# Kernel tuning notes

Measured on AMD Instinct MI355X. Metric: run time of the kernel, lower is better.

The kernel has to match this reference:

```python
import jax, jax.numpy as jnp
import numpy as np
import math

T = 120      # frame_num == audio_len == max_seq_len
D = 64       # hidden_layer_size
H = 2        # n_head
DH = D // H
DFF = 2 * D
DOUT = 31
PERIOD = 10
EPS = 1e-5
NEG = -1e9
SCALE = 1.0 / math.sqrt(DH)
SLOPES = (1.0 / 16.0, 1.0 / 256.0)  # ALiBi slopes for n_head=2


def _pe():
    # PeriodicPositionalEncoding: sinusoid over one period, tiled
    pos = jnp.arange(PERIOD, dtype=jnp.float32)[:, None]
    div = jnp.exp(jnp.arange(0, D, 2, dtype=jnp.float32) * (-math.log(10000.0) / D))
    s, c = jnp.sin(pos * div), jnp.cos(pos * div)
    pe = jnp.stack([s, c], axis=-1).reshape(PERIOD, D)  # interleave sin/cos
    return jnp.tile(pe, (T // PERIOD + 1, 1))[:T]


def _alibi_mask():
    # causal mask + ALiBi bias: alibi[i,j] = -slope * floor((i-j)/period) for j<=i
    slopes = jnp.array(SLOPES, dtype=jnp.float32)
    i = jnp.arange(T)[:, None]
    j = jnp.arange(T)[None, :]
    rel = ((i - j) // PERIOD).astype(jnp.float32)
    return jnp.where(j <= i, -slopes[:, None, None] * rel, NEG)  # [H,T,T]


def _ln(x, g, b):
    m = x.mean(-1, keepdims=True)
    v = ((x - m) ** 2).mean(-1, keepdims=True)
    return (x - m) / jnp.sqrt(v + EPS) * g + b


def setup_inputs() -> dict:
    key = jax.random.key(0)
    ks = iter(jax.random.split(key, 32))
    n = lambda shape, s=0.05: jax.random.normal(next(ks), shape, dtype=jnp.float32) * s
    inp = {
        'audio': jax.random.normal(next(ks), (1, T, 1024), dtype=jnp.float32),
        'W_audio': n((D, 1024)), 'b_audio': n((D,)),
        'obj_W': n((D, 5)),
        'Wq': n((D, D)), 'bq': n((D,)), 'Wk': n((D, D)), 'bk': n((D,)),
        'Wv': n((D, D)), 'bv': n((D,)), 'Wo': n((D, D)), 'bo': n((D,)),
        'Wv2': n((D, D)), 'bv2': n((D,)), 'Wo2': n((D, D)), 'bo2': n((D,)),
        'g1': jnp.ones((D,)), 'be1': jnp.zeros((D,)),
        'g2': jnp.ones((D,)), 'be2': jnp.zeros((D,)),
        'g3': jnp.ones((D,)), 'be3': jnp.zeros((D,)),
        'W1': n((DFF, D)), 'c1': n((DFF,)), 'W2': n((D, DFF)), 'c2': n((D,)),
        'Wr': n((DOUT, D)), 'br': n((DOUT,)), 'Wm': n((D, DOUT)), 'bm': n((D,)),
    }
    return inp


def _forward(audio, W_audio, b_audio, obj_W, Wq, bq, Wk, bk, Wv, bv, Wo, bo,
             Wv2, bv2, Wo2, bo2, g1, be1, g2, be2, g3, be3,
             W1, c1, W2, c2, Wr, br, Wm, bm):
    mem = audio[0] @ W_audio.T + b_audio          # [S,D], S == T
    style = obj_W[:, 0]                            # obj_vector @ [1,0,0,0,0]
    pe = _pe()
    mask = _alibi_mask()
    slopes = jnp.array(SLOPES, dtype=jnp.float32)
    jarr = jnp.arange(T)

    # enc_dec_mask leaves exactly one memory key per target row (anti-diagonal
    # from the end); the feedback row t at step t always attends memory[-1],
    # so its cross-attn output is just the projected value of the last frame.
    cross_last = (mem[-1] @ Wv2.T + bv2) @ Wo2.T + bo2  # [D]

    def step(emb, t):
        # decode only the last row (row t) of the growing sequence; 1-layer
        # post-norm decoder => row t depends only on input rows 0..t.
        x = emb + pe                                 # PPE over prefix
        xq = jnp.take(x, t, axis=0)                  # [D]
        q = (xq @ Wq.T + bq).reshape(H, DH)
        k = (x @ Wk.T + bk).reshape(T, H, DH)
        v = (x @ Wv.T + bv).reshape(T, H, DH)
        bias = jnp.where(jarr <= t,
                         -slopes[:, None] * ((t - jarr) // PERIOD).astype(jnp.float32),
                         NEG)                        # [H,T]
        sc = jnp.einsum('hd,shd->hs', q, k) * SCALE + bias
        a = jax.nn.softmax(sc, axis=-1)
        sa = jnp.einsum('hs,shd->hd', a, v).reshape(D) @ Wo.T + bo
        h1 = _ln(xq + sa, g1, be1)
        h2 = _ln(h1 + cross_last, g2, be2)
        h3 = _ln(h2 + jax.nn.relu(h2 @ W1.T + c1) @ W2.T + c2, g3, be3)
        new = (h3 @ Wr.T + br) @ Wm.T + bm + style   # vertice_map(vertice_map_r(.)) + style
        emb = jax.lax.dynamic_update_slice(emb, new[None, :], (t + 1, 0))
        return emb, None

    emb0 = jnp.zeros((T, D), audio.dtype).at[0].set(style)
    emb, _ = jax.lax.scan(step, emb0, jnp.arange(T - 1))

    # final full-length decode (last loop iteration of the torch module)
    x = emb + pe
    q = (x @ Wq.T + bq).reshape(T, H, DH)
    k = (x @ Wk.T + bk).reshape(T, H, DH)
    v = (x @ Wv.T + bv).reshape(T, H, DH)
    sc = jnp.einsum('thd,shd->hts', q, k) * SCALE + mask
    a = jax.nn.softmax(sc, axis=-1)
    sa = jnp.einsum('hts,shd->thd', a, v).reshape(T, D) @ Wo.T + bo
    h1 = _ln(x + sa, g1, be1)
    # at length T with S == T the enc_dec_mask aligns target row j <-> memory row j
    cross = (mem @ Wv2.T + bv2) @ Wo2.T + bo2
    h2 = _ln(h1 + cross, g2, be2)
    h3 = _ln(h2 + jax.nn.relu(h2 @ W1.T + c1) @ W2.T + c2, g3, be3)
    return (h3 @ Wr.T + br)[None]                    # [1,T,31]


def reference(audio, W_audio, b_audio, obj_W, Wq, bq, Wk, bk, Wv, bv, Wo, bo,
              Wv2, bv2, Wo2, bo2, g1, be1, g2, be2, g3, be3,
              W1, c1, W2, c2, Wr, br, Wm, bm):
    return _forward(audio, W_audio, b_audio, obj_W, Wq, bq, Wk, bk, Wv, bv, Wo, bo,
                    Wv2, bv2, Wo2, bo2, g1, be1, g2, be2, g3, be3,
                    W1, c1, W2, c2, Wr, br, Wm, bm)
```

## Files before the change

kernel.cpp:

```cpp
#include <hip/hip_runtime.h>

typedef unsigned short u16;
typedef unsigned int   u32;
typedef _Float16 f16;
typedef f16 h2 __attribute__((ext_vector_type(2)));
typedef f16 h4 __attribute__((ext_vector_type(4)));
typedef f16 h8 __attribute__((ext_vector_type(8)));

#define T_    120
#define D_    64
#define DOUT_ 31
#define KROW_ 68
#define VROW_ 132

#if defined(__has_builtin)
#if __has_builtin(__builtin_amdgcn_fdot2)
#define DOT2(a,b,c) __builtin_amdgcn_fdot2((a),(b),(c),false)
#endif
#endif
#ifndef DOT2
#define DOT2(a,b,c) ((float)(a).x*(float)(b).x + ((float)(a).y*(float)(b).y + (c)))
#endif
#define SHV(x,i,j) __builtin_shufflevector((x),(x),(i),(j))

__device__ __forceinline__ h2 pk(float a, float b){
#if defined(__has_builtin) && __has_builtin(__builtin_amdgcn_cvt_pkrtz)
  return __builtin_bit_cast(h2, __builtin_amdgcn_cvt_pkrtz(a, b));
#else
  h2 r; r.x = (f16)a; r.y = (f16)b; return r;
#endif
}
__device__ __forceinline__ float2 bp2(u32 u){
  float2 r; r.x = __uint_as_float(u << 16); r.y = __uint_as_float(u & 0xffff0000u); return r;
}
__device__ __forceinline__ u16 f2bu(float f){
  u32 u = __float_as_uint(f);
  u32 r = u + 0x7fffu + ((u >> 16) & 1u);
  return (u16)(r >> 16);
}
__device__ __forceinline__ u16 f2h16(float x){
  f16 v = (f16)x; u16 r; __builtin_memcpy(&r, &v, 2); return r;
}
__device__ __forceinline__ float fast_rcp(float x){
#if defined(__has_builtin) && __has_builtin(__builtin_amdgcn_rcpf)
  return __builtin_amdgcn_rcpf(x);
#else
  return 1.f / x;
#endif
}
#define WSYNC() do{ __asm__ __volatile__("" ::: "memory"); __builtin_amdgcn_wave_barrier(); }while(0)

__device__ __forceinline__ float dpp_sum(float x){
  int t;
  t = __builtin_amdgcn_update_dpp(0, __float_as_int(x), 0x111, 0xf, 0xf, true); x += __int_as_float(t);
  t = __builtin_amdgcn_update_dpp(0, __float_as_int(x), 0x112, 0xf, 0xf, true); x += __int_as_float(t);
  t = __builtin_amdgcn_update_dpp(0, __float_as_int(x), 0x114, 0xf, 0xf, true); x += __int_as_float(t);
  t = __builtin_amdgcn_update_dpp(0, __float_as_int(x), 0x118, 0xf, 0xf, true); x += __int_as_float(t);
  t = __builtin_amdgcn_update_dpp(0, __float_as_int(x), 0x142, 0xf, 0xf, true); x += __int_as_float(t);
  t = __builtin_amdgcn_update_dpp(0, __float_as_int(x), 0x143, 0xf, 0xf, true); x += __int_as_float(t);
  return __int_as_float(__builtin_amdgcn_readlane(__float_as_int(x), 63));
}
__device__ __forceinline__ float dpp_max_pos(float x){
  int t;
  t = __builtin_amdgcn_update_dpp(0, __float_as_int(x), 0x111, 0xf, 0xf, true); x = fmaxf(x, __int_as_float(t));
  t = __builtin_amdgcn_update_dpp(0, __float_as_int(x), 0x112, 0xf, 0xf, true); x = fmaxf(x, __int_as_float(t));
  t = __builtin_amdgcn_update_dpp(0, __float_as_int(x), 0x114, 0xf, 0xf, true); x = fmaxf(x, __int_as_float(t));
  t = __builtin_amdgcn_update_dpp(0, __float_as_int(x), 0x118, 0xf, 0xf, true); x = fmaxf(x, __int_as_float(t));
  t = __builtin_amdgcn_update_dpp(0, __float_as_int(x), 0x142, 0xf, 0xf, true); x = fmaxf(x, __int_as_float(t));
  t = __builtin_amdgcn_update_dpp(0, __float_as_int(x), 0x143, 0xf, 0xf, true); x = fmaxf(x, __int_as_float(t));
  return __int_as_float(__builtin_amdgcn_readlane(__float_as_int(x), 63));
}
__device__ __forceinline__ float pe_val(int row, int i){
  const float coef = -0.28782313662425574f;
  int p = row % 10;
  float dv  = __expf((float)(i >> 1) * coef);
  float ang = (float)p * dv;
  return (i & 1) ? __cosf(ang) : __sinf(ang);
}
__device__ __forceinline__ void loadrow32(h2* dst, const float* row){
  #pragma unroll
  for (int r = 0; r < 16; ++r){
    float4 f = ((const float4*)row)[r];
    dst[2*r]   = pk(f.x, f.y);
    dst[2*r+1] = pk(f.z, f.w);
  }
}

__global__ __launch_bounds__(256) void k_pre0(const float* __restrict__ audio,
                                              const float* __restrict__ Wa, const float* __restrict__ ba,
                                              const float* __restrict__ Wv2, const float* __restrict__ bv2,
                                              const float* __restrict__ Wo2, const float* __restrict__ bo2,
                                              const float* __restrict__ Wo, const float* __restrict__ W1,
                                              const float* __restrict__ W2, const float* __restrict__ Wr,
                                              const float* __restrict__ Wm, const float* __restrict__ br,
                                              const float* __restrict__ bm,
                                              float* __restrict__ cross, float* __restrict__ Ms,
                                              float* __restrict__ bMv,
                                              u16* __restrict__ wob, u16* __restrict__ w1b,
                                              u16* __restrict__ w2b, u16* __restrict__ wrb){
  const int tid = threadIdx.x;
  __shared__ float ash[1024];
  __shared__ float msh[64], tsh[64];
  for (int i = tid; i < 1024; i += 256) ash[i] = audio[119*1024 + i];
  for (int i = tid; i < 4096; i += 256) wob[i] = f2bu(Wo[i]);
  for (int i = tid; i < 8192; i += 256){ w1b[i] = f2bu(W1[i]); w2b[i] = f2bu(W2[i]); }
  for (int i = tid; i < 1984; i += 256) wrb[i] = f2bu(Wr[i]);
  for (int idx = tid; idx < 4096; idx += 256){
    int d = idx >> 6, e = idx & 63;
    float acc = 0.f;
    #pragma unroll
    for (int j = 0; j < 31; ++j) acc += Wm[d*31 + j] * Wr[j*64 + e];
    Ms[idx] = acc;
  }
  if (tid < 64){
    float acc = bm[tid];
    #pragma unroll
    for (int j = 0; j < 31; ++j) acc += Wm[tid*31 + j] * br[j];
    bMv[tid] = acc;
  }
  __syncthreads();
  const int w = tid >> 6, lane = tid & 63;
  for (int d = w*16; d < w*16 + 16; ++d){
    const float4* row = (const float4*)(Wa + d*1024);
    float acc = 0.f;
    #pragma unroll
    for (int m = 0; m < 4; ++m){
      float4 wp = row[lane + 64*m];
      int j = 4*(lane + 64*m);
      acc += wp.x*ash[j] + wp.y*ash[j+1] + wp.z*ash[j+2] + wp.w*ash[j+3];
    }
    acc = dpp_sum(acc);
    if (lane == 0) msh[d] = acc + ba[d];
  }
  __syncthreads();
  if (tid < 64){
    const float4* r1 = (const float4*)(Wv2 + tid*64);
    float a = bv2[tid];
    #pragma unroll
    for (int j = 0; j < 16; ++j){ float4 p = r1[j]; a += p.x*msh[4*j] + p.y*msh[4*j+1] + p.z*msh[4*j+2] + p.w*msh[4*j+3]; }
    tsh[tid] = a;
  }
  __syncthreads();
  if (tid < 64){
    const float4* r2 = (const float4*)(Wo2 + tid*64);
    float c = bo2[tid];
    #pragma unroll
    for (int j = 0; j < 16; ++j){ float4 p = r2[j]; c += p.x*tsh[4*j] + p.y*tsh[4*j+1] + p.z*tsh[4*j+2] + p.w*tsh[4*j+3]; }
    cross[119*64 + tid] = c;
  }
}

__global__ __launch_bounds__(128, 1) void k_main(
    const float* __restrict__ audio,
    const float* __restrict__ Wa, const float* __restrict__ ba,
    const float* __restrict__ Wv2, const float* __restrict__ bv2,
    const float* __restrict__ Wo2, const float* __restrict__ bo2,
    const float* __restrict__ objW,
    const float* __restrict__ Wq, const float* __restrict__ bq,
    const float* __restrict__ Wk, const float* __restrict__ bk,
    const float* __restrict__ Wv, const float* __restrict__ bv,
    const float* __restrict__ Wo, const float* __restrict__ bo,
    const float* __restrict__ g1, const float* __restrict__ be1,
    const float* __restrict__ g2, const float* __restrict__ be2,
    const float* __restrict__ g3, const float* __restrict__ be3,
    const float* __restrict__ W1, const float* __restrict__ c1,
    const float* __restrict__ W2, const float* __restrict__ c2,
    const float* __restrict__ Ms, const float* __restrict__ bMv,
    float* __restrict__ cross,
    u16* __restrict__ xw16, u16* __restrict__ Kw16, u16* __restrict__ Vw16)
{
  __shared__ __align__(16) f16 KcS[128*KROW_];
  __shared__ __align__(16) f16 VcS[D_*VROW_];
  __shared__ __align__(16) f16 xwS[T_*D_];
  __shared__ __align__(16) f16 sch[256];
  __shared__ __align__(16) f16 xh[64], qh[64], h2h[64], h3h[64];
  __shared__ __align__(16) f16 at2h[64];
  __shared__ __align__(16) f16 fsh[128];
  __shared__ float pP0[64], pP1[64];
  __shared__ float ivP[2];
  __shared__ float pe_tab[640];

  const int tid = threadIdx.x;

  if (blockIdx.x != 119){
    float* ash = (float*)KcS;
    float* msh = (float*)VcS;
    float* tsh = msh + 64;
    const int b = blockIdx.x;
    for (int idx = tid; idx < 1024; idx += 128) ash[idx] = audio[b*1024 + idx];
    __syncthreads();
    const int w = tid >> 6, lane = tid & 63;
    for (int d = w*32; d < w*32 + 32; ++d){
      const float4* row = (const float4*)(Wa + d*1024);
      float acc = 0.f;
      #pragma unroll
      for (int m = 0; m < 4; ++m){
        float4 wp = row[lane + 64*m];
        int j = 4*(lane + 64*m);
        acc += wp.x*ash[j] + wp.y*ash[j+1] + wp.z*ash[j+2] + wp.w*ash[j+3];
      }
      acc = dpp_sum(acc);
      if (lane == 0) msh[d] = acc + ba[d];
    }
    __syncthreads();
    if (tid < 64){
      const float4* r1 = (const float4*)(Wv2 + tid*64);
      float a = bv2[tid];
      #pragma unroll
      for (int j = 0; j < 16; ++j){ float4 p = r1[j]; a += p.x*msh[4*j] + p.y*msh[4*j+1] + p.z*msh[4*j+2] + p.w*msh[4*j+3]; }
      tsh[tid] = a;
    }
    __syncthreads();
    if (tid < 64){
      const float4* r2 = (const float4*)(Wo2 + tid*64);
      float c = bo2[tid];
      #pragma unroll
      for (int j = 0; j < 16; ++j){ float4 p = r2[j]; c += p.x*tsh[4*j] + p.y*tsh[4*j+1] + p.z*tsh[4*j+2] + p.w*tsh[4*j+3]; }
      cross[b*64 + tid] = c;
    }
    return;
  }

  const int i = tid & 63;
  const int hh = tid >> 6;
  const bool w1w = hh != 0;

  h2 A[32], B[32], C[32], D[32], G[32], E[32];
  float biasA=0.f, biasB=0.f, bo_r=0.f, c1r=0.f, c2_r=0.f, cls_r=0.f;
  float g1r=0.f,b1r=0.f,g2r=0.f,b2r=0.f;
  float mg_r=0.f, u_r=0.f;
  float x_r;

  {
    const int qi = hh*32 + (i & 31);
    if (i < 32){ loadrow32(A, Wq + qi*64); biasA = bq[qi]; }
    else       { loadrow32(A, Wk + qi*64); biasA = bk[qi]; }
    loadrow32(B, Wv + qi*64);  biasB = bv[qi];
    loadrow32(C, Wo + i*64);
    loadrow32(D, W1 + (hh*64 + i)*64);
    loadrow32(G, W2 + i*128 + hh*64);
    {
      const float4* mr  = (const float4*)(Ms + i*64);
      const float4* gv  = (const float4*)g3;
      const float4* b3v = (const float4*)be3;
      float mg = 0.f, mb = 0.f;
      #pragma unroll
      for (int r = 0; r < 16; ++r){
        float4 f = mr[r], g = gv[r], b = b3v[r];
        float e0 = f.x*g.x, e1 = f.y*g.y, e2 = f.z*g.z, e3 = f.w*g.w;
        E[2*r]   = pk(e0, e1);
        E[2*r+1] = pk(e2, e3);
        mg += (e0+e1)+(e2+e3);
        mb += f.x*b.x + f.y*b.y + f.z*b.z + f.w*b.w;
      }
      mg_r = mg;
      u_r  = bMv[i] + objW[i*5] + mb;
    }
    c1r = c1[hh*64 + i]; c2_r = c2[i]; bo_r = bo[i];
    g1r = g1[i]; b1r = be1[i]; g2r = g2[i]; b2r = be2[i];
    cls_r = cross[119*64 + i];
  }
  { u32* p = (u32*)KcS; for (int idx = tid; idx < 128*KROW_/2; idx += 128) p[idx] = 0; }
  { u32* p = (u32*)VcS; for (int idx = tid; idx < D_*VROW_/2;  idx += 128) p[idx] = 0; }
  for (int idx = tid; idx < 640; idx += 128) pe_tab[idx] = pe_val(idx >> 6, idx & 63);
  {
    float x0 = objW[i*5] + pe_val(0, i);
    x_r = x0;
    xh[i] = (f16)x0;
    if (w1w) xwS[i] = (f16)x0;
  }
  __syncthreads();

  int pp = 1;
  const float slope = hh ? 0.00390625f : 0.0625f;
  for (int t = 0; t < T_-1; ++t){
    float e0r, e1r;
    h8 xr[8];
    {
      const h8* xv = (const h8*)xh;
      #pragma unroll
      for (int r = 0; r < 8; ++r) xr[r] = xv[r];
      float a0=biasA,a1=0.f,a2=0.f,a3=0.f;
      #pragma unroll
      for (int r = 0; r < 8; ++r){
        h8 x = xr[r];
        a0 = DOT2(A[4*r+0], SHV(x,0,1), a0);
        a1 = DOT2(A[4*r+1], SHV(x,2,3), a1);
        a2 = DOT2(A[4*r+2], SHV(x,4,5), a2);
        a3 = DOT2(A[4*r+3], SHV(x,6,7), a3);
      }
      float qk = (a0+a1)+(a2+a3);
      f16* dst = (i < 32) ? (qh + hh*32 + i) : (KcS + t*KROW_ + hh*32 + (i - 32));
      *dst = (f16)qk;
    }
    WSYNC();
    {
      if (i < 32){
        float v0=biasB,v1=0.f,v2=0.f,v3=0.f;
        #pragma unroll
        for (int r = 0; r < 8; ++r){
          h8 x = xr[r];
          v0 = DOT2(B[4*r+0], SHV(x,0,1), v0); v1 = DOT2(B[4*r+1], SHV(x,2,3), v1);
          v2 = DOT2(B[4*r+2], SHV(x,4,5), v2); v3 = DOT2(B[4*r+3], SHV(x,6,7), v3);
        }
        VcS[(hh*32 + i)*VROW_ + t] = (f16)((v0+v1)+(v2+v3));
      }
      const int j = i;
      const h8* qv = (const h8*)(qh + hh*32);
      const h4* k0 = (const h4*)(KcS + j*KROW_ + hh*32);
      const h4* k1 = (const h4*)(KcS + (j+64)*KROW_ + hh*32);
      float d0a=0.f,d0b=0.f,d1a=0.f,d1b=0.f;
      #pragma unroll
      for (int r = 0; r < 4; ++r){
        h8 q = qv[r];
        h4 ka = k0[2*r], kb = k0[2*r+1], kc = k1[2*r], kd = k1[2*r+1];
        d0a = DOT2(SHV(ka,0,1), SHV(q,0,1), d0a);
        d0b = DOT2(SHV(ka,2,3), SHV(q,2,3), d0b);
        d0a = DOT2(SHV(kb,0,1), SHV(q,4,5), d0a);
        d0b = DOT2(SHV(kb,2,3), SHV(q,6,7), d0b);
        d1a = DOT2(SHV(kc,0,1), SHV(q,0,1), d1a);
        d1b = DOT2(SHV(kc,2,3), SHV(q,2,3), d1b);
        d1a = DOT2(SHV(kd,0,1), SHV(q,4,5), d1a);
        d1b = DOT2(SHV(kd,2,3), SHV(q,6,7), d1b);
      }
      float d0 = d0a + d0b, d1 = d1a + d1b;
      int r0 = (t - j) / 10, r1 = (t - j - 64) / 10;
      float s0 = d0*0.17677669529663687f - slope*(float)r0;
      float s1 = d1*0.17677669529663687f - slope*(float)r1;
      e0r = (j      <= t) ? __expf(fminf(s0, 8.f)) : 0.f;
      e1r = (j + 64 <= t) ? __expf(fminf(s1, 8.f)) : 0.f;
      sch[hh*128 + j]      = (f16)e0r;
      sch[hh*128 + j + 64] = (f16)e1r;
    }
    WSYNC();
    {
      float den = dpp_sum(e0r + e1r);
      float inv_w = fast_rcp(den);
      if (i == 0) ivP[hh] = inv_w;
      const int l5 = i & 31;
      const int d  = hh*32 + l5;
      const int co = (i & 32) ? 64 : 0;
      const h8* av = (const h8*)(sch + hh*128 + co);
      const h4* vv = (const h4*)(VcS + d*VROW_ + co);
      float p0=0.f,p1=0.f,p2=0.f,p3=0.f;
      #pragma unroll
      for (int r = 0; r < 8; ++r){
        h8 a = av[r];
        h4 va = vv[2*r], vb = vv[2*r+1];
        p0 = DOT2(SHV(va,0,1), SHV(a,0,1), p0);
        p1 = DOT2(SHV(va,2,3), SHV(a,2,3), p1);
        p2 = DOT2(SHV(vb,0,1), SHV(a,4,5), p2);
        p3 = DOT2(SHV(vb,2,3), SHV(a,6,7), p3);
      }
      float p = (p0+p1)+(p2+p3);
      p += __shfl_xor(p, 32, 64);
      at2h[hh*32 + l5] = (f16)p;
    }
    __syncthreads();
    float h2v;
    {
      float inv0 = ivP[0], inv1 = ivP[1];
      const h8* pv = (const h8*)at2h;
      float l0=0.f,l1=0.f,q0=0.f,q1=0.f;
      #pragma unroll
      for (int r = 0; r < 4; ++r){
        h8 x = pv[r];
        l0 = DOT2(C[4*r+0], SHV(x,0,1), l0); l1 = DOT2(C[4*r+1], SHV(x,2,3), l1);
        l0 = DOT2(C[4*r+2], SHV(x,4,5), l0); l1 = DOT2(C[4*r+3], SHV(x,6,7), l1);
      }
      #pragma unroll
      for (int r = 4; r < 8; ++r){
        h8 x = pv[r];
        q0 = DOT2(C[4*r+0], SHV(x,0,1), q0); q1 = DOT2(C[4*r+1], SHV(x,2,3), q1);
        q0 = DOT2(C[4*r+2], SHV(x,4,5), q0); q1 = DOT2(C[4*r+3], SHV(x,6,7), q1);
      }
      float sa = bo_r + inv0*(l0+l1) + inv1*(q0+q1);
      float y = x_r + sa;
      float s = dpp_sum(y), s2 = dpp_sum(y*y);
      float m = s*(1.f/64.f), var = fmaxf(s2*(1.f/64.f) - m*m, 0.f);
      float h1 = (y - m)*rsqrtf(var + 1e-5f)*g1r + b1r;
      float z = h1 + cls_r;
      float sz = dpp_sum(z), sz2 = dpp_sum(z*z);
      float mz = sz*(1.f/64.f), vz = fmaxf(sz2*(1.f/64.f) - mz*mz, 0.f);
      h2v = (z - mz)*rsqrtf(vz + 1e-5f)*g2r + b2r;
      h2h[i] = (f16)h2v;
      WSYNC();
      const h8* hv = (const h8*)h2h;
      float a0=c1r, a1=0.f, a2=0.f, a3=0.f;
      #pragma unroll
      for (int r = 0; r < 8; ++r){
        h8 x = hv[r];
        a0 = DOT2(D[4*r+0], SHV(x,0,1), a0);
        a1 = DOT2(D[4*r+1], SHV(x,2,3), a1);
        a2 = DOT2(D[4*r+2], SHV(x,4,5), a2);
        a3 = DOT2(D[4*r+3], SHV(x,6,7), a3);
      }
      fsh[hh*64 + i] = (f16)fmaxf((a0+a1)+(a2+a3), 0.f);
      WSYNC();
      const h8* fv = (const h8*)(fsh + hh*64);
      float f0=0.f, f1=0.f, f2=0.f, f3=0.f;
      #pragma unroll
      for (int r = 0; r < 8; ++r){
        h8 x = fv[r];
        f0 = DOT2(G[4*r+0], SHV(x,0,1), f0);
        f1 = DOT2(G[4*r+1], SHV(x,2,3), f1);
        f2 = DOT2(G[4*r+2], SHV(x,4,5), f2);
        f3 = DOT2(G[4*r+3], SHV(x,6,7), f3);
      }
      float* pP = hh ? pP1 : pP0;
      pP[i] = (f0+f1)+(f2+f3);
    }
    __syncthreads();
    {
      float y3 = h2v + c2_r + pP0[i] + pP1[i];
      h3h[i] = (f16)y3;
      WSYNC();
      const h8* yv3 = (const h8*)h3h;
      h8 yr[8];
      #pragma unroll
      for (int r = 0; r < 8; ++r) yr[r] = yv3[r];
      float s3 = dpp_sum(y3), s32 = dpp_sum(y3*y3);
      float m3 = s3*(1.f/64.f), v3 = fmaxf(s32*(1.f/64.f) - m3*m3, 0.f);
      float invs = rsqrtf(v3 + 1e-5f);
      float m0=0.f, m1=0.f, m2=0.f, mm3=0.f;
      #pragma unroll
      for (int r = 0; r < 8; ++r){
        h8 x = yr[r];
        m0 = DOT2(E[4*r+0], SHV(x,0,1), m0);
        m1 = DOT2(E[4*r+1], SHV(x,2,3), m1);
        m2 = DOT2(E[4*r+2], SHV(x,4,5), m2);
        mm3 = DOT2(E[4*r+3], SHV(x,6,7), mm3);
      }
      float xn = ((m0+m1)+(m2+mm3))*invs + (u_r - m3*invs*mg_r) + pe_tab[pp*64 + i];
      x_r = xn;
      xh[i] = (f16)xn;
      if (w1w) xwS[(t+1)*64 + i] = (f16)xn;
    }
    WSYNC();
    pp = (pp == 9) ? 0 : pp + 1;
  }
  {
    const h8* xv = (const h8*)xh;
    h8 xr[8];
    #pragma unroll
    for (int r = 0; r < 8; ++r) xr[r] = xv[r];
    if (i < 32){
      float v0=biasB,v1=0.f,v2=0.f,v3=0.f;
      #pragma unroll
      for (int r = 0; r < 8; ++r){
        h8 x = xr[r];
        v0 = DOT2(B[4*r+0], SHV(x,0,1), v0);
        v1 = DOT2(B[4*r+1], SHV(x,2,3), v1);
        v2 = DOT2(B[4*r+2], SHV(x,4,5), v2);
        v3 = DOT2(B[4*r+3], SHV(x,6,7), v3);
      }
      Vw16[119*64 + hh*32 + i] = f2h16((v0+v1)+(v2+v3));
    } else {
      float k0=biasA,k1=0.f,k2=0.f,k3=0.f;
      #pragma unroll
      for (int r = 0; r < 8; ++r){
        h8 x = xr[r];
        k0 = DOT2(A[4*r+0], SHV(x,0,1), k0);
        k1 = DOT2(A[4*r+1], SHV(x,2,3), k1);
        k2 = DOT2(A[4*r+2], SHV(x,4,5), k2);
        k3 = DOT2(A[4*r+3], SHV(x,6,7), k3);
      }
      Kw16[119*64 + hh*32 + (i-32)] = f2h16((k0+k1)+(k2+k3));
    }
  }
  __syncthreads();
  {
    const u16* kc = (const u16*)KcS;
    const u16* vc = (const u16*)VcS;
    for (int idx = tid; idx < 119*64; idx += 128){
      int t_ = idx >> 6, d = idx & 63;
      Kw16[idx] = kc[t_*KROW_ + d];
      Vw16[idx] = vc[d*VROW_ + t_];
    }
    const u32* xs32 = (const u32*)xwS;
    for (int idx = tid; idx < T_*D_/2; idx += 128) ((u32*)xw16)[idx] = xs32[idx];
  }
}

__global__ __launch_bounds__(128) void k_final(
    const float* __restrict__ Wq, const float* __restrict__ bq, const float* __restrict__ bo,
    const float* __restrict__ g1, const float* __restrict__ be1,
    const float* __restrict__ g2, const float* __restrict__ be2,
    const float* __restrict__ g3, const float* __restrict__ be3,
    const float* __restrict__ c1, const float* __restrict__ c2, const float* __restrict__ br,
    const u16* __restrict__ wo_b, const u16* __restrict__ w1_b,
    const u16* __restrict__ w2_b, const u16* __restrict__ wr_b,
    const float* __restrict__ cross, const u16* __restrict__ xw16,
    const u16* __restrict__ Kw16, const u16* __restrict__ Vw16,
    float* __restrict__ out)
{
  __shared__ float xs[64], qs[64], at[64], h2s[64], h3s[64], fs[128], sc[256];
  const int irow = blockIdx.x, tid = threadIdx.x;
  const f16* xp = (const f16*)xw16;
  const f16* kp = (const f16*)Kw16;
  const f16* vp = (const f16*)Vw16;
  if (tid < 64) xs[tid] = (float)xp[irow*64 + tid];
  __syncthreads();
  if (tid < 64){
    const float4* wr_ = (const float4*)(Wq + tid*64);
    float acc = bq[tid];
    #pragma unroll
    for (int j = 0; j < 16; ++j){ float4 w = wr_[j]; acc += w.x*xs[4*j] + w.y*xs[4*j+1] + w.z*xs[4*j+2] + w.w*xs[4*j+3]; }
    qs[tid] = acc;
  }
  __syncthreads();
  {
    const int h = tid >> 6, j = tid & 63;
    const float* qh_ = qs + h*32;
    float d0 = 0.f, d1 = 0.f;
    const h4* k0 = (const h4*)(kp + j*64 + h*32);
    #pragma unroll
    for (int w = 0; w < 8; ++w){
      h4 p = k0[w];
      d0 += (float)p.x*qh_[4*w] + (float)p.y*qh_[4*w+1] + (float)p.z*qh_[4*w+2] + (float)p.w*qh_[4*w+3];
    }
    if (j < 56){
      const h4* k1 = (const h4*)(kp + (j+64)*64 + h*32);
      #pragma unroll
      for (int w = 0; w < 8; ++w){
        h4 p = k1[w];
        d1 += (float)p.x*qh_[4*w] + (float)p.y*qh_[4*w+1] + (float)p.z*qh_[4*w+2] + (float)p.w*qh_[4*w+3];
      }
    }
    const float slope = h ? 0.00390625f : 0.0625f;
    float s0 = (j      <= irow) ? d0*0.17677669529663687f - slope*(float)((irow-j)/10)    : -1e30f;
    float s1 = (j + 64 <= irow) ? d1*0.17677669529663687f - slope*(float)((irow-j-64)/10) : -1e30f;
    float m = dpp_max_pos(fmaxf(s0, s1) + 16384.f) - 16384.f;
    float e0 = (j      <= irow) ? __expf(s0 - m) : 0.f;
    float e1 = (j + 64 <= irow) ? __expf(s1 - m) : 0.f;
    float inv = 1.f / dpp_sum(e0 + e1);
    sc[h*128 + j]      = e0*inv;
    sc[h*128 + j + 64] = e1*inv;
  }
  __syncthreads();
  if (tid < 64){
    const float* a = sc + (tid >> 5)*128;
    float a0=0.f,a1=0.f,a2=0.f,a3=0.f;
    #pragma unroll
    for (int jj = 0; jj < 30; ++jj){
      a0 += a[4*jj]   * (float)vp[(4*jj)*64   + tid];
      a1 += a[4*jj+1] * (float)vp[(4*jj+1)*64 + tid];
      a2 += a[4*jj+2] * (float)vp[(4*jj+2)*64 + tid];
      a3 += a[4*jj+3] * (float)vp[(4*jj+3)*64 + tid];
    }
    at[tid] = (a0+a1)+(a2+a3);
  }
  __syncthreads();
  if (tid < 64){
    const u32* orow = (const u32*)(wo_b + tid*64);
    float acc = bo[tid];
    #pragma unroll
    for (int w = 0; w < 32; ++w){ float2 p = bp2(orow[w]); acc += p.x*at[2*w] + p.y*at[2*w+1]; }
    float y = xs[tid] + acc;
    float s = dpp_sum(y), s2 = dpp_sum(y*y);
    float m = s*(1.f/64.f), var = fmaxf(s2*(1.f/64.f) - m*m, 0.f);
    float h1 = (y - m)*rsqrtf(var + 1e-5f)*g1[tid] + be1[tid];
    float z = h1 + cross[irow*64 + tid];
    float sz = dpp_sum(z), sz2 = dpp_sum(z*z);
    float mz = sz*(1.f/64.f), vz = fmaxf(sz2*(1.f/64.f) - mz*mz, 0.f);
    h2s[tid] = (z - mz)*rsqrtf(vz + 1e-5f)*g2[tid] + be2[tid];
  }
  __syncthreads();
  {
    const u32* w1r = (const u32*)(w1_b + tid*64);
    float acc = c1[tid];
    #pragma unroll
    for (int w = 0; w < 32; ++w){ float2 p = bp2(w1r[w]); acc += p.x*h2s[2*w] + p.y*h2s[2*w+1]; }
    fs[tid] = fmaxf(acc, 0.f);
  }
  __syncthreads();
  if (tid < 64){
    const u32* w2r = (const u32*)(w2_b + tid*128);
    float acc = c2[tid];
    #pragma unroll
    for (int w = 0; w < 64; ++w){ float2 p = bp2(w2r[w]); acc += p.x*fs[2*w] + p.y*fs[2*w+1]; }
    float y = h2s[tid] + acc;
    float s = dpp_sum(y), s2 = dpp_sum(y*y);
    float m = s*(1.f/64.f), var = fmaxf(s2*(1.f/64.f) - m*m, 0.f);
    h3s[tid] = (y - m)*rsqrtf(var + 1e-5f)*g3[tid] + be3[tid];
  }
  __syncthreads();
  if (tid < DOUT_){
    const u32* rr = (const u32*)(wr_b + tid*64);
    float acc = br[tid];
    #pragma unroll
    for (int w = 0; w < 32; ++w){ float2 p = bp2(rr[w]); acc += p.x*h3s[2*w] + p.y*h3s[2*w+1]; }
    out[irow*DOUT_ + tid] = acc;
  }
}

extern "C" void kernel_launch(void* const* d_in, const int* in_sizes, int n_in,
                              void* d_out, int out_size, void* d_ws, size_t ws_size,
                              hipStream_t stream){
  const float* audio=(const float*)d_in[0];
  const float* Wa   =(const float*)d_in[1];
  const float* ba   =(const float*)d_in[2];
  const float* objW =(const float*)d_in[3];
  const float* Wq   =(const float*)d_in[4];
  const float* bq   =(const float*)d_in[5];
  const float* Wk   =(const float*)d_in[6];
  const float* bk   =(const float*)d_in[7];
  const float* Wv   =(const float*)d_in[8];
  const float* bv   =(const float*)d_in[9];
  const float* Wo   =(const float*)d_in[10];
  const float* bo   =(const float*)d_in[11];
  const float* Wv2  =(const float*)d_in[12];
  const float* bv2  =(const float*)d_in[13];
  const float* Wo2  =(const float*)d_in[14];
  const float* bo2  =(const float*)d_in[15];
  const float* g1   =(const float*)d_in[16];
  const float* be1  =(const float*)d_in[17];
  const float* g2   =(const float*)d_in[18];
  const float* be2  =(const float*)d_in[19];
  const float* g3   =(const float*)d_in[20];
  const float* be3  =(const float*)d_in[21];
  const float* W1   =(const float*)d_in[22];
  const float* c1   =(const float*)d_in[23];
  const float* W2   =(const float*)d_in[24];
  const float* c2   =(const float*)d_in[25];
  const float* Wr   =(const float*)d_in[26];
  const float* br   =(const float*)d_in[27];
  const float* Wm   =(const float*)d_in[28];
  const float* bm   =(const float*)d_in[29];

  float* ws    = (float*)d_ws;
  float* cross = ws;
  float* Ms    = ws + 7680;
  float* bMv   = ws + 11776;
  u16* xw16 = (u16*)(ws + 11840);
  u16* Kw16 = xw16 + 7680;
  u16* Vw16 = Kw16 + 7680;
  u16* wo_b = Vw16 + 7680;
  u16* w1_b = wo_b + 4096;
  u16* w2_b = w1_b + 8192;
  u16* wr_b = w2_b + 8192;
  float* out = (float*)d_out;

  k_pre0 <<<dim3(1),   dim3(256), 0, stream>>>(audio, Wa, ba, Wv2, bv2, Wo2, bo2,
                                               Wo, W1, W2, Wr, Wm, br, bm,
                                               cross, Ms, bMv, wo_b, w1_b, w2_b, wr_b);
  k_main <<<dim3(120), dim3(128), 0, stream>>>(audio, Wa, ba, Wv2, bv2, Wo2, bo2,
                                               objW, Wq, bq, Wk, bk, Wv, bv, Wo, bo,
                                               g1, be1, g2, be2, g3, be3,
                                               W1, c1, W2, c2, Ms, bMv,
                                               cross, xw16, Kw16, Vw16);
  k_final<<<dim3(120), dim3(128), 0, stream>>>(Wq, bq, bo, g1, be1, g2, be2, g3, be3,
                                               c1, c2, br, wo_b, w1_b, w2_b, wr_b,
                                               cross, xw16, Kw16, Vw16, out);
}
```

Baseline: 381.1 us.

## Fold prep kernel into single-block scan and compute cross rows in final kernel

Removes the separate single-block prep kernel. Its weight conversion, Wm·Wr folding and last-row cross computation move into the single-block scan kernel's prologue. The 119 cross-attention rows that were computed by extra blocks of the main kernel are now computed per row inside the final kernel. The FFN second layer is no longer split across both waves with a partial-sum reduction; each wave holds the full W2 row in registers. This drops one launch and the global cross/Ms buffers, but it lengthens the serial prologue of the scan, where the weight conversion and Wm·Wr product now run on only 128 threads, and it raises register pressure.

```diff
diff --git a/kernel.cpp b/kernel.cpp
--- a/kernel.cpp
+++ b/kernel.cpp
@@ -86,71 +86,7 @@
   }
 }
 
-__global__ __launch_bounds__(256) void k_pre0(const float* __restrict__ audio,
-                                              const float* __restrict__ Wa, const float* __restrict__ ba,
-                                              const float* __restrict__ Wv2, const float* __restrict__ bv2,
-                                              const float* __restrict__ Wo2, const float* __restrict__ bo2,
-                                              const float* __restrict__ Wo, const float* __restrict__ W1,
-                                              const float* __restrict__ W2, const float* __restrict__ Wr,
-                                              const float* __restrict__ Wm, const float* __restrict__ br,
-                                              const float* __restrict__ bm,
-                                              float* __restrict__ cross, float* __restrict__ Ms,
-                                              float* __restrict__ bMv,
-                                              u16* __restrict__ wob, u16* __restrict__ w1b,
-                                              u16* __restrict__ w2b, u16* __restrict__ wrb){
-  const int tid = threadIdx.x;
-  __shared__ float ash[1024];
-  __shared__ float msh[64], tsh[64];
-  for (int i = tid; i < 1024; i += 256) ash[i] = audio[119*1024 + i];
-  for (int i = tid; i < 4096; i += 256) wob[i] = f2bu(Wo[i]);
-  for (int i = tid; i < 8192; i += 256){ w1b[i] = f2bu(W1[i]); w2b[i] = f2bu(W2[i]); }
-  for (int i = tid; i < 1984; i += 256) wrb[i] = f2bu(Wr[i]);
-  for (int idx = tid; idx < 4096; idx += 256){
-    int d = idx >> 6, e = idx & 63;
-    float acc = 0.f;
-    #pragma unroll
-    for (int j = 0; j < 31; ++j) acc += Wm[d*31 + j] * Wr[j*64 + e];
-    Ms[idx] = acc;
-  }
-  if (tid < 64){
-    float acc = bm[tid];
-    #pragma unroll
-    for (int j = 0; j < 31; ++j) acc += Wm[tid*31 + j] * br[j];
-    bMv[tid] = acc;
-  }
-  __syncthreads();
-  const int w = tid >> 6, lane = tid & 63;
-  for (int d = w*16; d < w*16 + 16; ++d){
-    const float4* row = (const float4*)(Wa + d*1024);
-    float acc = 0.f;
-    #pragma unroll
-    for (int m = 0; m < 4; ++m){
-      float4 wp = row[lane + 64*m];
-      int j = 4*(lane + 64*m);
-      acc += wp.x*ash[j] + wp.y*ash[j+1] + wp.z*ash[j+2] + wp.w*ash[j+3];
-    }
-    acc = dpp_sum(acc);
-    if (lane == 0) msh[d] = acc + ba[d];
-  }
-  __syncthreads();
-  if (tid < 64){
-    const float4* r1 = (const float4*)(Wv2 + tid*64);
-    float a = bv2[tid];
-    #pragma unroll
-    for (int j = 0; j < 16; ++j){ float4 p = r1[j]; a += p.x*msh[4*j] + p.y*msh[4*j+1] + p.z*msh[4*j+2] + p.w*msh[4*j+3]; }
-    tsh[tid] = a;
-  }
-  __syncthreads();
-  if (tid < 64){
-    const float4* r2 = (const float4*)(Wo2 + tid*64);
-    float c = bo2[tid];
-    #pragma unroll
-    for (int j = 0; j < 16; ++j){ float4 p = r2[j]; c += p.x*tsh[4*j] + p.y*tsh[4*j+1] + p.z*tsh[4*j+2] + p.w*tsh[4*j+3]; }
-    cross[119*64 + tid] = c;
-  }
-}
-
-__global__ __launch_bounds__(128, 1) void k_main(
+__global__ __launch_bounds__(128, 1) void k_scan(
     const float* __restrict__ audio,
     const float* __restrict__ Wa, const float* __restrict__ ba,
     const float* __restrict__ Wv2, const float* __restrict__ bv2,
@@ -165,9 +101,11 @@
     const float* __restrict__ g3, const float* __restrict__ be3,
     const float* __restrict__ W1, const float* __restrict__ c1,
     const float* __restrict__ W2, const float* __restrict__ c2,
-    const float* __restrict__ Ms, const float* __restrict__ bMv,
-    float* __restrict__ cross,
-    u16* __restrict__ xw16, u16* __restrict__ Kw16, u16* __restrict__ Vw16)
+    const float* __restrict__ Wm, const float* __restrict__ br,
+    const float* __restrict__ bm, const float* __restrict__ Wr,
+    u16* __restrict__ xw16, u16* __restrict__ Kw16, u16* __restrict__ Vw16,
+    u16* __restrict__ wob, u16* __restrict__ w1b,
+    u16* __restrict__ w2b, u16* __restrict__ wrb)
 {
   __shared__ __align__(16) f16 KcS[128*KROW_];
   __shared__ __align__(16) f16 VcS[D_*VROW_];
@@ -176,31 +114,42 @@
   __shared__ __align__(16) f16 xh[64], qh[64], h2h[64], h3h[64];
   __shared__ __align__(16) f16 at2h[64];
   __shared__ __align__(16) f16 fsh[128];
-  __shared__ float pP0[64], pP1[64];
   __shared__ float ivP[2];
   __shared__ float pe_tab[640];
 
   const int tid = threadIdx.x;
-
-  if (blockIdx.x != 119){
+  const int i = tid & 63;
+  const int hh = tid >> 6;
+  const bool w1w = hh != 0;
+
+  h2 A[32], B[32], C[32], D[32], G[64], E[32];
+  float biasA=0.f, biasB=0.f, bo_r=0.f, c1r=0.f, c2_r=0.f, cls_r=0.f;
+  float g1r=0.f,b1r=0.f,g2r=0.f,b2r=0.f;
+  float mg_r=0.f, u_r=0.f;
+  float x_r;
+
+  {
+    for (int idx = tid; idx < 4096; idx += 128) wob[idx] = f2bu(Wo[idx]);
+    for (int idx = tid; idx < 8192; idx += 128){ w1b[idx] = f2bu(W1[idx]); w2b[idx] = f2bu(W2[idx]); }
+    for (int idx = tid; idx < 1984; idx += 128) wrb[idx] = f2bu(Wr[idx]);
     float* ash = (float*)KcS;
     float* msh = (float*)VcS;
     float* tsh = msh + 64;
-    const int b = blockIdx.x;
-    for (int idx = tid; idx < 1024; idx += 128) ash[idx] = audio[b*1024 + idx];
+    float* wrL = (float*)xwS;
+    for (int idx = tid; idx < 1024; idx += 128) ash[idx] = audio[119*1024 + idx];
+    for (int idx = tid; idx < 1984; idx += 128) wrL[idx] = Wr[idx];
     __syncthreads();
-    const int w = tid >> 6, lane = tid & 63;
-    for (int d = w*32; d < w*32 + 32; ++d){
+    for (int d = hh*32; d < hh*32 + 32; ++d){
       const float4* row = (const float4*)(Wa + d*1024);
       float acc = 0.f;
       #pragma unroll
       for (int m = 0; m < 4; ++m){
-        float4 wp = row[lane + 64*m];
-        int j = 4*(lane + 64*m);
+        float4 wp = row[i + 64*m];
+        int j = 4*(i + 64*m);
         acc += wp.x*ash[j] + wp.y*ash[j+1] + wp.z*ash[j+2] + wp.w*ash[j+3];
       }
       acc = dpp_sum(acc);
-      if (lane == 0) msh[d] = acc + ba[d];
+      if (i == 0) msh[d] = acc + ba[d];
     }
     __syncthreads();
     if (tid < 64){
@@ -211,25 +160,42 @@
       tsh[tid] = a;
     }
     __syncthreads();
-    if (tid < 64){
-      const float4* r2 = (const float4*)(Wo2 + tid*64);
-      float c = bo2[tid];
+    {
+      const float4* r2 = (const float4*)(Wo2 + i*64);
+      float c = bo2[i];
       #pragma unroll
       for (int j = 0; j < 16; ++j){ float4 p = r2[j]; c += p.x*tsh[4*j] + p.y*tsh[4*j+1] + p.z*tsh[4*j+2] + p.w*tsh[4*j+3]; }
-      cross[b*64 + tid] = c;
-    }
-    return;
-  }
-
-  const int i = tid & 63;
-  const int hh = tid >> 6;
-  const bool w1w = hh != 0;
-
-  h2 A[32], B[32], C[32], D[32], G[32], E[32];
-  float biasA=0.f, biasB=0.f, bo_r=0.f, c1r=0.f, c2_r=0.f, cls_r=0.f;
-  float g1r=0.f,b1r=0.f,g2r=0.f,b2r=0.f;
-  float mg_r=0.f, u_r=0.f;
-  float x_r;
+      cls_r = c;
+    }
+    {
+      float wm[31];
+      #pragma unroll
+      for (int j = 0; j < 31; ++j) wm[j] = Wm[i*31 + j];
+      float mg = 0.f, mb = 0.f, bsum = 0.f;
+      const float4* gv  = (const float4*)g3;
+      const float4* b3v = (const float4*)be3;
+      #pragma unroll
+      for (int q = 0; q < 16; ++q){
+        float ax=0.f, ay=0.f, az=0.f, aw=0.f;
+        #pragma unroll
+        for (int j = 0; j < 31; ++j){
+          float4 wr4 = ((const float4*)(wrL + j*64))[q];
+          ax += wm[j]*wr4.x; ay += wm[j]*wr4.y; az += wm[j]*wr4.z; aw += wm[j]*wr4.w;
+        }
+        float4 g = gv[q], b = b3v[q];
+        float e0 = ax*g.x, e1 = ay*g.y, e2 = az*g.z, e3 = aw*g.w;
+        E[2*q]   = pk(e0, e1);
+        E[2*q+1] = pk(e2, e3);
+        mg += (e0+e1)+(e2+e3);
+        mb += ax*b.x + ay*b.y + az*b.z + aw*b.w;
+      }
+      mg_r = mg;
+      #pragma unroll
+      for (int j = 0; j < 31; ++j) bsum += wm[j]*br[j];
+      u_r = bm[i] + bsum + objW[i*5] + mb;
+    }
+    __syncthreads();
+  }
 
   {
     const int qi = hh*32 + (i & 31);
@@ -238,27 +204,10 @@
     loadrow32(B, Wv + qi*64);  biasB = bv[qi];
     loadrow32(C, Wo + i*64);
     loadrow32(D, W1 + (hh*64 + i)*64);
-    loadrow32(G, W2 + i*128 + hh*64);
-    {
-      const float4* mr  = (const float4*)(Ms + i*64);
-      const float4* gv  = (const float4*)g3;
-      const float4* b3v = (const float4*)be3;
-      float mg = 0.f, mb = 0.f;
-      #pragma unroll
-      for (int r = 0; r < 16; ++r){
-        float4 f = mr[r], g = gv[r], b = b3v[r];
-        float e0 = f.x*g.x, e1 = f.y*g.y, e2 = f.z*g.z, e3 = f.w*g.w;
-        E[2*r]   = pk(e0, e1);
-        E[2*r+1] = pk(e2, e3);
-        mg += (e0+e1)+(e2+e3);
-        mb += f.x*b.x + f.y*b.y + f.z*b.z + f.w*b.w;
-      }
-      mg_r = mg;
-      u_r  = bMv[i] + objW[i*5] + mb;
-    }
+    loadrow32(G,      W2 + i*128);
+    loadrow32(G + 32, W2 + i*128 + 64);
     c1r = c1[hh*64 + i]; c2_r = c2[i]; bo_r = bo[i];
     g1r = g1[i]; b1r = be1[i]; g2r = g2[i]; b2r = be2[i];
-    cls_r = cross[119*64 + i];
   }
   { u32* p = (u32*)KcS; for (int idx = tid; idx < 128*KROW_/2; idx += 128) p[idx] = 0; }
   { u32* p = (u32*)VcS; for (int idx = tid; idx < D_*VROW_/2;  idx += 128) p[idx] = 0; }
@@ -396,23 +345,20 @@
         a3 = DOT2(D[4*r+3], SHV(x,6,7), a3);
       }
       fsh[hh*64 + i] = (f16)fmaxf((a0+a1)+(a2+a3), 0.f);
-      WSYNC();
-      const h8* fv = (const h8*)(fsh + hh*64);
-      float f0=0.f, f1=0.f, f2=0.f, f3=0.f;
-      #pragma unroll
-      for (int r = 0; r < 8; ++r){
+    }
+    __syncthreads();
+    {
+      const h8* fv = (const h8*)fsh;
+      float f0=c2_r, f1=0.f, f2=0.f, f3=0.f;
+      #pragma unroll
+      for (int r = 0; r < 16; ++r){
         h8 x = fv[r];
         f0 = DOT2(G[4*r+0], SHV(x,0,1), f0);
         f1 = DOT2(G[4*r+1], SHV(x,2,3), f1);
         f2 = DOT2(G[4*r+2], SHV(x,4,5), f2);
         f3 = DOT2(G[4*r+3], SHV(x,6,7), f3);
       }
-      float* pP = hh ? pP1 : pP0;
-      pP[i] = (f0+f1)+(f2+f3);
-    }
-    __syncthreads();
-    {
-      float y3 = h2v + c2_r + pP0[i] + pP1[i];
+      float y3 = h2v + (f0+f1)+(f2+f3);
       h3h[i] = (f16)y3;
       WSYNC();
       const h8* yv3 = (const h8*)h3h;
@@ -483,6 +429,10 @@
 }
 
 __global__ __launch_bounds__(128) void k_final(
+    const float* __restrict__ audio,
+    const float* __restrict__ Wa, const float* __restrict__ ba,
+    const float* __restrict__ Wv2, const float* __restrict__ bv2,
+    const float* __restrict__ Wo2, const float* __restrict__ bo2,
     const float* __restrict__ Wq, const float* __restrict__ bq, const float* __restrict__ bo,
     const float* __restrict__ g1, const float* __restrict__ be1,
     const float* __restrict__ g2, const float* __restrict__ be2,
@@ -490,16 +440,49 @@
     const float* __restrict__ c1, const float* __restrict__ c2, const float* __restrict__ br,
     const u16* __restrict__ wo_b, const u16* __restrict__ w1_b,
     const u16* __restrict__ w2_b, const u16* __restrict__ wr_b,
-    const float* __restrict__ cross, const u16* __restrict__ xw16,
-    const u16* __restrict__ Kw16, const u16* __restrict__ Vw16,
+    const u16* __restrict__ xw16, const u16* __restrict__ Kw16, const u16* __restrict__ Vw16,
     float* __restrict__ out)
 {
+  __shared__ float ash[1024], msh[64], tsh[64], crs[64];
   __shared__ float xs[64], qs[64], at[64], h2s[64], h3s[64], fs[128], sc[256];
   const int irow = blockIdx.x, tid = threadIdx.x;
   const f16* xp = (const f16*)xw16;
   const f16* kp = (const f16*)Kw16;
   const f16* vp = (const f16*)Vw16;
+  for (int idx = tid; idx < 1024; idx += 128) ash[idx] = audio[irow*1024 + idx];
   if (tid < 64) xs[tid] = (float)xp[irow*64 + tid];
+  __syncthreads();
+  {
+    const int w = tid >> 6, lane = tid & 63;
+    for (int d = w*32; d < w*32 + 32; ++d){
+      const float4* row = (const float4*)(Wa + d*1024);
+      float acc = 0.f;
+      #pragma unroll
+      for (int m = 0; m < 4; ++m){
+        float4 wp = row[lane + 64*m];
+        int j = 4*(lane + 64*m);
+        acc += wp.x*ash[j] + wp.y*ash[j+1] + wp.z*ash[j+2] + wp.w*ash[j+3];
+      }
+      acc = dpp_sum(acc);
+      if (lane == 0) msh[d] = acc + ba[d];
+    }
+  }
+  __syncthreads();
+  if (tid < 64){
+    const float4* r1 = (const float4*)(Wv2 + tid*64);
+    float a = bv2[tid];
+    #pragma unroll
+    for (int j = 0; j < 16; ++j){ float4 p = r1[j]; a += p.x*msh[4*j] + p.y*msh[4*j+1] + p.z*msh[4*j+2] + p.w*msh[4*j+3]; }
+    tsh[tid] = a;
+  }
+  __syncthreads();
+  if (tid < 64){
+    const float4* r2 = (const float4*)(Wo2 + tid*64);
+    float c = bo2[tid];
+    #pragma unroll
+    for (int j = 0; j < 16; ++j){ float4 p = r2[j]; c += p.x*tsh[4*j] + p.y*tsh[4*j+1] + p.z*tsh[4*j+2] + p.w*tsh[4*j+3]; }
+    crs[tid] = c;
+  }
   __syncthreads();
   if (tid < 64){
     const float4* wr_ = (const float4*)(Wq + tid*64);
@@ -560,7 +543,7 @@
     float s = dpp_sum(y), s2 = dpp_sum(y*y);
     float m = s*(1.f/64.f), var = fmaxf(s2*(1.f/64.f) - m*m, 0.f);
     float h1 = (y - m)*rsqrtf(var + 1e-5f)*g1[tid] + be1[tid];
-    float z = h1 + cross[irow*64 + tid];
+    float z = h1 + crs[tid];
     float sz = dpp_sum(z), sz2 = dpp_sum(z*z);
     float mz = sz*(1.f/64.f), vz = fmaxf(sz2*(1.f/64.f) - mz*mz, 0.f);
     h2s[tid] = (z - mz)*rsqrtf(vz + 1e-5f)*g2[tid] + be2[tid];
@@ -628,11 +611,7 @@
   const float* Wm   =(const float*)d_in[28];
   const float* bm   =(const float*)d_in[29];
 
-  float* ws    = (float*)d_ws;
-  float* cross = ws;
-  float* Ms    = ws + 7680;
-  float* bMv   = ws + 11776;
-  u16* xw16 = (u16*)(ws + 11840);
+  u16* xw16 = (u16*)d_ws;
   u16* Kw16 = xw16 + 7680;
   u16* Vw16 = Kw16 + 7680;
   u16* wo_b = Vw16 + 7680;
@@ -641,15 +620,14 @@
   u16* wr_b = w2_b + 8192;
   float* out = (float*)d_out;
 
-  k_pre0 <<<dim3(1),   dim3(256), 0, stream>>>(audio, Wa, ba, Wv2, bv2, Wo2, bo2,
-                                               Wo, W1, W2, Wr, Wm, br, bm,
-                                               cross, Ms, bMv, wo_b, w1_b, w2_b, wr_b);
-  k_main <<<dim3(120), dim3(128), 0, stream>>>(audio, Wa, ba, Wv2, bv2, Wo2, bo2,
+  k_scan <<<dim3(1),   dim3(128), 0, stream>>>(audio, Wa, ba, Wv2, bv2, Wo2, bo2,
                                                objW, Wq, bq, Wk, bk, Wv, bv, Wo, bo,
                                                g1, be1, g2, be2, g3, be3,
-                                               W1, c1, W2, c2, Ms, bMv,
-                                               cross, xw16, Kw16, Vw16);
-  k_final<<<dim3(120), dim3(128), 0, stream>>>(Wq, bq, bo, g1, be1, g2, be2, g3, be3,
+                                               W1, c1, W2, c2, Wm, br, bm, Wr,
+                                               xw16, Kw16, Vw16,
+                                               wo_b, w1_b, w2_b, wr_b);
+  k_final<<<dim3(120), dim3(128), 0, stream>>>(audio, Wa, ba, Wv2, bv2, Wo2, bo2,
+                                               Wq, bq, bo, g1, be1, g2, be2, g3, be3,
                                                c1, c2, br, wo_b, w1_b, w2_b, wr_b,
-                                               cross, xw16, Kw16, Vw16, out);
-}
+                                               xw16, Kw16, Vw16, out);
+}
```

After: 466.8 us. +22.5%, slower.
